# Performance work log

Hardware: AMD Instinct MI355X
Metric: run time of the kernel (lower is better)

The kernel has to match this reference:

```python
import jax, jax.numpy as jnp
import numpy as np
import math

D_MODEL = 1024
N_HEADS = 16
D_K = D_MODEL // N_HEADS
B, L = 4, 2048


def setup_inputs() -> dict:
    key = jax.random.key(0)
    ks = jax.random.split(key, 11)
    s = 1.0 / math.sqrt(D_MODEL)
    inp = {
        "queries": jax.random.normal(ks[0], (B, L, D_MODEL), jnp.float32),
        "keys": jax.random.normal(ks[1], (B, L, D_MODEL), jnp.float32),
        "values": jax.random.normal(ks[2], (B, L, D_MODEL), jnp.float32),
        "Wq": jax.random.normal(ks[3], (D_MODEL, D_MODEL), jnp.float32) * s,
        "bq": jax.random.normal(ks[4], (D_MODEL,), jnp.float32) * s,
        "Wk": jax.random.normal(ks[5], (D_MODEL, D_MODEL), jnp.float32) * s,
        "bk": jax.random.normal(ks[6], (D_MODEL,), jnp.float32) * s,
        "Wv": jax.random.normal(ks[7], (D_MODEL, D_MODEL), jnp.float32) * s,
        "bv": jax.random.normal(ks[8], (D_MODEL,), jnp.float32) * s,
        "Wo": jax.random.normal(ks[9], (D_MODEL, D_MODEL), jnp.float32) * s,
        "bo": jax.random.normal(ks[10], (D_MODEL,), jnp.float32) * s,
    }
    return inp


def _heads(x):
    b, l, _ = x.shape
    return x.reshape(b, l, N_HEADS, D_K).transpose(0, 2, 1, 3)  # (B,H,L,Dk)


def reference(queries, keys, values, Wq, bq, Wk, bk, Wv, bv, Wo, bo):
    Q = _heads(queries @ Wq.T + bq)
    K = _heads(keys @ Wk.T + bk)
    V = _heads(values @ Wv.T + bv)
    scores = jnp.einsum("bhqd,bhkd->bhqk", Q, K) / math.sqrt(D_K)
    t = jnp.arange(L, dtype=scores.dtype)
    time_bias = -0.1 * jnp.abs(t[None, :] - t[:, None])  # (L,L)
    attn = jax.nn.softmax(scores + time_bias[None, None], axis=-1)
    out = jnp.einsum("bhqk,bhkd->bhqd", attn, V)
    out = out.transpose(0, 2, 1, 3).reshape(queries.shape[0], L, D_MODEL)
    return out @ Wo.T + bo
```

## Files before the change

### kernel.cpp

```cpp
#include <hip/hip_runtime.h>
#include <hip/hip_bf16.h>
#include <stdint.h>

typedef __bf16 bf16x8 __attribute__((ext_vector_type(8)));
typedef float f32x4 __attribute__((ext_vector_type(4)));

__device__ __forceinline__ uint16_t f2bf(float f){
  uint32_t u = __builtin_bit_cast(uint32_t, f);
  u += 0x7fffu + ((u >> 16) & 1u);
  return (uint16_t)(u >> 16);
}

__device__ __forceinline__ void gld_lds16(const void* g, void* l){
  __builtin_amdgcn_global_load_lds((const __attribute__((address_space(1))) void*)g,
                                   (__attribute__((address_space(3))) void*)l, 16, 0, 0);
}

__global__ void convert_f32_bf16(const float* __restrict__ s, uint16_t* __restrict__ d, int n4){
  int i = blockIdx.x * blockDim.x + threadIdx.x;
  if (i >= n4) return;
  float4 v = ((const float4*)s)[i];
  ushort4 o;
  o.x = f2bf(v.x); o.y = f2bf(v.y); o.z = f2bf(v.z); o.w = f2bf(v.w);
  ((ushort4*)d)[i] = o;
}

__launch_bounds__(256, 2)
__global__ void gemm_bt(const uint16_t* __restrict__ A, const uint16_t* __restrict__ W,
                        const float* __restrict__ bias, void* __restrict__ out, int mode,
                        float oscale)
{
  __shared__ uint16_t As[128 * 64];
  __shared__ uint16_t Ws[128 * 64];
  const int tid = threadIdx.x;
  const int wave = tid >> 6, lane = tid & 63;
  const int g = lane >> 4, li = lane & 15;
  const int m0 = blockIdx.x * 128, n0 = blockIdx.y * 128;
  const int wr = (wave >> 1) * 64, wc = (wave & 1) * 64;

  f32x4 acc[4][4];
#pragma unroll
  for (int m = 0; m < 4; m++)
#pragma unroll
    for (int n = 0; n < 4; n++) acc[m][n] = f32x4{0.f, 0.f, 0.f, 0.f};

  const uint16_t* Asrc[4];
  const uint16_t* Wsrc[4];
  int cid[4];
#pragma unroll
  for (int j = 0; j < 4; j++) {
    cid[j] = j * 256 + tid;
    int row = cid[j] >> 3, c = cid[j] & 7;
    int sc = c ^ (row & 7);
    Asrc[j] = A + (size_t)(m0 + row) * 1024 + sc * 8;
    Wsrc[j] = W + (size_t)(n0 + row) * 1024 + sc * 8;
  }

  for (int k0 = 0; k0 < 1024; k0 += 64) {
#pragma unroll
    for (int j = 0; j < 4; j++) {
      gld_lds16(Asrc[j] + k0, (char*)As + cid[j] * 16);
      gld_lds16(Wsrc[j] + k0, (char*)Ws + cid[j] * 16);
    }
    __syncthreads();

#pragma unroll
    for (int kh = 0; kh < 2; kh++) {
      bf16x8 a[4], bfr[4];
#pragma unroll
      for (int m = 0; m < 4; m++) {
        int row = wr + m * 16 + li;
        int ch = (kh * 4 + g) ^ (row & 7);
        a[m] = *(const bf16x8*)((const char*)As + row * 128 + ch * 16);
      }
#pragma unroll
      for (int n = 0; n < 4; n++) {
        int row = wc + n * 16 + li;
        int ch = (kh * 4 + g) ^ (row & 7);
        bfr[n] = *(const bf16x8*)((const char*)Ws + row * 128 + ch * 16);
      }
#pragma unroll
      for (int m = 0; m < 4; m++)
#pragma unroll
        for (int n = 0; n < 4; n++)
          acc[m][n] = __builtin_amdgcn_mfma_f32_16x16x32_bf16(a[m], bfr[n], acc[m][n], 0, 0, 0);
    }
    __syncthreads();
  }

  if (mode == 0) {
    uint16_t* O = (uint16_t*)out;
#pragma unroll
    for (int n = 0; n < 4; n++) {
      int col = n0 + wc + n * 16 + li;
      float bv = bias[col];
#pragma unroll
      for (int m = 0; m < 4; m++) {
        int row = m0 + wr + m * 16 + g * 4;
#pragma unroll
        for (int r = 0; r < 4; r++)
          O[(size_t)(row + r) * 1024 + col] = f2bf((acc[m][n][r] + bv) * oscale);
      }
    }
  } else if (mode == 2) {
    uint16_t* O = (uint16_t*)out;
#pragma unroll
    for (int n = 0; n < 4; n++) {
      int col = n0 + wc + n * 16 + li;
      float bv = bias[col];
#pragma unroll
      for (int m = 0; m < 4; m++) {
        int mg = m0 + wr + m * 16 + g * 4;
        int bidx = mg >> 11;
        int l = mg & 2047;
        ushort4 pk;
        pk.x = f2bf(acc[m][n][0] + bv);
        pk.y = f2bf(acc[m][n][1] + bv);
        pk.z = f2bf(acc[m][n][2] + bv);
        pk.w = f2bf(acc[m][n][3] + bv);
        *(ushort4*)(O + ((size_t)bidx * 1024 + col) * 2048 + l) = pk;
      }
    }
  } else {
    float* O = (float*)out;
#pragma unroll
    for (int n = 0; n < 4; n++) {
      int col = n0 + wc + n * 16 + li;
      float bv = bias[col];
#pragma unroll
      for (int m = 0; m < 4; m++) {
        int row = m0 + wr + m * 16 + g * 4;
#pragma unroll
        for (int r = 0; r < 4; r++)
          O[(size_t)(row + r) * 1024 + col] = acc[m][n][r] + bv;
      }
    }
  }
}

__launch_bounds__(256, 2)
__global__ void flash_attn(const uint16_t* __restrict__ Qw, const uint16_t* __restrict__ Kw,
                           const uint16_t* __restrict__ Vt, uint16_t* __restrict__ Ow)
{
  __shared__ uint16_t Ks[64 * 64];
  __shared__ uint16_t Vs[64 * 64];
  __shared__ uint16_t Ps[4][16 * 64];

  const float C2 = 0.14426950408889635f;
  const float C3 = 20.1977305724455f;

  const int tid = threadIdx.x;
  const int wave = tid >> 6, lane = tid & 63;
  const int g = lane >> 4, li = lane & 15;
  const int q0 = blockIdx.x * 64;
  const int bh = blockIdx.y;
  const int b = bh >> 4, h = bh & 15;

  const uint16_t* Qp = Qw + (size_t)(b * 2048 + q0 + wave * 16 + li) * 1024 + h * 64 + g * 8;
  bf16x8 qf0 = *(const bf16x8*)Qp;
  bf16x8 qf1 = *(const bf16x8*)(Qp + 32);

  float l_r[4] = {0.f, 0.f, 0.f, 0.f};
  f32x4 o[4];
#pragma unroll
  for (int nd = 0; nd < 4; nd++) o[nd] = f32x4{0.f, 0.f, 0.f, 0.f};

  const int cid0 = tid, cid1 = 256 + tid;
  const int kr0 = cid0 >> 3, c0 = cid0 & 7;
  const int kr1 = cid1 >> 3, c1 = cid1 & 7;
  const int sc0 = c0 ^ (kr0 & 7), sc1 = c1 ^ (kr1 & 7);

  const uint16_t* Kb0 = Kw + (size_t)(b * 2048 + kr0) * 1024 + h * 64 + sc0 * 8;
  const uint16_t* Kb1 = Kw + (size_t)(b * 2048 + kr1) * 1024 + h * 64 + sc1 * 8;
  const uint16_t* Vb0 = Vt + (size_t)(bh * 64 + kr0) * 2048 + sc0 * 8;
  const uint16_t* Vb1 = Vt + (size_t)(bh * 64 + kr1) * 2048 + sc1 * 8;

  const int kv_lo = (q0 >= 256) ? (q0 - 256) : 0;
  const int kv_hi = (q0 + 320 <= 2048) ? (q0 + 320) : 2048;
  const int tq0 = q0 + wave * 16 + g * 4;

  for (int kv0 = kv_lo; kv0 < kv_hi; kv0 += 64) {
    gld_lds16(Kb0 + (size_t)kv0 * 1024, (char*)Ks + cid0 * 16);
    gld_lds16(Kb1 + (size_t)kv0 * 1024, (char*)Ks + cid1 * 16);
    gld_lds16(Vb0 + kv0, (char*)Vs + cid0 * 16);
    gld_lds16(Vb1 + kv0, (char*)Vs + cid1 * 16);
    __syncthreads();

    float p[4][4];
#pragma unroll
    for (int n = 0; n < 4; n++) {
      int kr = n * 16 + li;
      bf16x8 bk0 = *(const bf16x8*)((const char*)Ks + kr * 128 + ((g ^ (kr & 7)) << 4));
      bf16x8 bk1 = *(const bf16x8*)((const char*)Ks + kr * 128 + (((4 + g) ^ (kr & 7)) << 4));
      f32x4 s = f32x4{0.f, 0.f, 0.f, 0.f};
      s = __builtin_amdgcn_mfma_f32_16x16x32_bf16(qf0, bk0, s, 0, 0, 0);
      s = __builtin_amdgcn_mfma_f32_16x16x32_bf16(qf1, bk1, s, 0, 0, 0);
      float dtb = (float)(tq0 - (kv0 + n * 16 + li));
#pragma unroll
      for (int r = 0; r < 4; r++) {
        float e = exp2f((s[r] - C3) - C2 * fabsf(dtb + (float)r));
        p[n][r] = e;
        l_r[r] += e;
      }
    }

#pragma unroll
    for (int n = 0; n < 4; n++)
#pragma unroll
      for (int r = 0; r < 4; r++) {
        int prow = g * 4 + r;
        int c = n * 16 + li;
        Ps[wave][prow * 64 + ((((c >> 3) ^ (prow & 7))) << 3) + (c & 7)] = f2bf(p[n][r]);
      }

    bf16x8 pa0 = *(const bf16x8*)((const char*)Ps[wave] + li * 128 + ((g ^ (li & 7)) << 4));
    bf16x8 pa1 = *(const bf16x8*)((const char*)Ps[wave] + li * 128 + (((4 + g) ^ (li & 7)) << 4));
#pragma unroll
    for (int nd = 0; nd < 4; nd++) {
      int vr = nd * 16 + li;
      bf16x8 vb0 = *(const bf16x8*)((const char*)Vs + vr * 128 + ((g ^ (vr & 7)) << 4));
      bf16x8 vb1 = *(const bf16x8*)((const char*)Vs + vr * 128 + (((4 + g) ^ (vr & 7)) << 4));
      o[nd] = __builtin_amdgcn_mfma_f32_16x16x32_bf16(pa0, vb0, o[nd], 0, 0, 0);
      o[nd] = __builtin_amdgcn_mfma_f32_16x16x32_bf16(pa1, vb1, o[nd], 0, 0, 0);
    }
    __syncthreads();
  }

#pragma unroll
  for (int r = 0; r < 4; r++) {
    float l = l_r[r];
    l += __shfl_xor(l, 1);
    l += __shfl_xor(l, 2);
    l += __shfl_xor(l, 4);
    l += __shfl_xor(l, 8);
    float inv = 1.0f / l;
    int qg = b * 2048 + q0 + wave * 16 + g * 4 + r;
#pragma unroll
    for (int nd = 0; nd < 4; nd++)
      Ow[(size_t)qg * 1024 + h * 64 + nd * 16 + li] = f2bf(o[nd][r] * inv);
  }
}

extern "C" void kernel_launch(void* const* d_in, const int* in_sizes, int n_in,
                              void* d_out, int out_size, void* d_ws, size_t ws_size,
                              hipStream_t stream) {
  const float* q  = (const float*)d_in[0];
  const float* k  = (const float*)d_in[1];
  const float* v  = (const float*)d_in[2];
  const float* Wq = (const float*)d_in[3];
  const float* bq = (const float*)d_in[4];
  const float* Wk = (const float*)d_in[5];
  const float* bk = (const float*)d_in[6];
  const float* Wv = (const float*)d_in[7];
  const float* bv = (const float*)d_in[8];
  const float* Wo = (const float*)d_in[9];
  const float* bo = (const float*)d_in[10];

  const size_t NX = (size_t)8192 * 1024;
  const size_t NW = (size_t)1024 * 1024;

  uint16_t* Xb  = (uint16_t*)d_ws;
  uint16_t* Wb  = Xb + NX;
  uint16_t* Vtw = Wb + NW;
  uint16_t* Aws = Xb;
  uint16_t* Qws = (uint16_t*)d_out;
  uint16_t* Kws = Qws + NX;

  const int n4x = (int)(NX / 4);
  const int n4w = (int)(NW / 4);

  dim3 ggrid(64, 8);
  const float qscale = 0.18033688011112042f;

  convert_f32_bf16<<<n4x / 256, 256, 0, stream>>>(q, Xb, n4x);
  convert_f32_bf16<<<n4w / 256, 256, 0, stream>>>(Wq, Wb, n4w);
  gemm_bt<<<ggrid, 256, 0, stream>>>(Xb, Wb, bq, Qws, 0, qscale);

  convert_f32_bf16<<<n4x / 256, 256, 0, stream>>>(k, Xb, n4x);
  convert_f32_bf16<<<n4w / 256, 256, 0, stream>>>(Wk, Wb, n4w);
  gemm_bt<<<ggrid, 256, 0, stream>>>(Xb, Wb, bk, Kws, 0, 1.0f);

  convert_f32_bf16<<<n4x / 256, 256, 0, stream>>>(v, Xb, n4x);
  convert_f32_bf16<<<n4w / 256, 256, 0, stream>>>(Wv, Wb, n4w);
  gemm_bt<<<ggrid, 256, 0, stream>>>(Xb, Wb, bv, Vtw, 2, 1.0f);

  flash_attn<<<dim3(32, 64), 256, 0, stream>>>(Qws, Kws, Vtw, Aws);

  convert_f32_bf16<<<n4w / 256, 256, 0, stream>>>(Wo, Wb, n4w);
  gemm_bt<<<ggrid, 256, 0, stream>>>(Aws, Wb, bo, d_out, 3, 1.0f);
}
```

Baseline: 313.6 us.

## Double-buffer GEMM LDS tiles and merge input/weight conversion launches

The GEMM now keeps two LDS buffers per operand and issues the global-to-LDS loads for the next K tile before computing on the current one. The aim is to overlap load latency with MFMA work and drop one barrier per iteration. Activation and weight f32-to-bf16 conversions are merged into a single launch to save launch overhead, and the manual rounding is replaced by the compiler's bf16 cast. Doubling LDS use may lower occupancy. With only one barrier per iteration, there is also a risk of overwriting the buffer still being read from the previous iteration, since no wait or barrier is visible before the next prefetch.

```diff
diff --git a/kernel.cpp b/kernel.cpp
--- a/kernel.cpp
+++ b/kernel.cpp
@@ -6,9 +6,8 @@
 typedef float f32x4 __attribute__((ext_vector_type(4)));
 
 __device__ __forceinline__ uint16_t f2bf(float f){
-  uint32_t u = __builtin_bit_cast(uint32_t, f);
-  u += 0x7fffu + ((u >> 16) & 1u);
-  return (uint16_t)(u >> 16);
+  __bf16 h = (__bf16)f;
+  return __builtin_bit_cast(uint16_t, h);
 }
 
 __device__ __forceinline__ void gld_lds16(const void* g, void* l){
@@ -16,9 +15,12 @@
                                    (__attribute__((address_space(3))) void*)l, 16, 0, 0);
 }
 
-__global__ void convert_f32_bf16(const float* __restrict__ s, uint16_t* __restrict__ d, int n4){
+__global__ void convert2(const float* __restrict__ s1, uint16_t* __restrict__ d1, int n4_1,
+                         const float* __restrict__ s2, uint16_t* __restrict__ d2, int n4_2){
   int i = blockIdx.x * blockDim.x + threadIdx.x;
-  if (i >= n4) return;
+  const float* s; uint16_t* d;
+  if (i < n4_1) { s = s1; d = d1; }
+  else { i -= n4_1; if (i >= n4_2) return; s = s2; d = d2; }
   float4 v = ((const float4*)s)[i];
   ushort4 o;
   o.x = f2bf(v.x); o.y = f2bf(v.y); o.z = f2bf(v.z); o.w = f2bf(v.w);
@@ -30,8 +32,8 @@
                         const float* __restrict__ bias, void* __restrict__ out, int mode,
                         float oscale)
 {
-  __shared__ uint16_t As[128 * 64];
-  __shared__ uint16_t Ws[128 * 64];
+  __shared__ uint16_t As[2][128 * 64];
+  __shared__ uint16_t Ws[2][128 * 64];
   const int tid = threadIdx.x;
   const int wave = tid >> 6, lane = tid & 63;
   const int g = lane >> 4, li = lane & 15;
@@ -56,14 +58,27 @@
     Wsrc[j] = W + (size_t)(n0 + row) * 1024 + sc * 8;
   }
 
-  for (int k0 = 0; k0 < 1024; k0 += 64) {
-#pragma unroll
-    for (int j = 0; j < 4; j++) {
-      gld_lds16(Asrc[j] + k0, (char*)As + cid[j] * 16);
-      gld_lds16(Wsrc[j] + k0, (char*)Ws + cid[j] * 16);
-    }
-    __syncthreads();
-
+#pragma unroll
+  for (int j = 0; j < 4; j++) {
+    gld_lds16(Asrc[j], (char*)As[0] + cid[j] * 16);
+    gld_lds16(Wsrc[j], (char*)Ws[0] + cid[j] * 16);
+  }
+  __syncthreads();
+
+  for (int t = 0; t < 16; t++) {
+    const int cur = t & 1;
+    if (t < 15) {
+      const int k1 = (t + 1) * 64;
+      const int nxt = cur ^ 1;
+#pragma unroll
+      for (int j = 0; j < 4; j++) {
+        gld_lds16(Asrc[j] + k1, (char*)As[nxt] + cid[j] * 16);
+        gld_lds16(Wsrc[j] + k1, (char*)Ws[nxt] + cid[j] * 16);
+      }
+    }
+
+    const char* Ab = (const char*)As[cur];
+    const char* Wb = (const char*)Ws[cur];
 #pragma unroll
     for (int kh = 0; kh < 2; kh++) {
       bf16x8 a[4], bfr[4];
@@ -71,13 +86,13 @@
       for (int m = 0; m < 4; m++) {
         int row = wr + m * 16 + li;
         int ch = (kh * 4 + g) ^ (row & 7);
-        a[m] = *(const bf16x8*)((const char*)As + row * 128 + ch * 16);
+        a[m] = *(const bf16x8*)(Ab + row * 128 + ch * 16);
       }
 #pragma unroll
       for (int n = 0; n < 4; n++) {
         int row = wc + n * 16 + li;
         int ch = (kh * 4 + g) ^ (row & 7);
-        bfr[n] = *(const bf16x8*)((const char*)Ws + row * 128 + ch * 16);
+        bfr[n] = *(const bf16x8*)(Wb + row * 128 + ch * 16);
       }
 #pragma unroll
       for (int m = 0; m < 4; m++)
@@ -268,24 +283,22 @@
 
   const int n4x = (int)(NX / 4);
   const int n4w = (int)(NW / 4);
+  const int gcv = (n4x + n4w) / 256;
 
   dim3 ggrid(64, 8);
   const float qscale = 0.18033688011112042f;
 
-  convert_f32_bf16<<<n4x / 256, 256, 0, stream>>>(q, Xb, n4x);
-  convert_f32_bf16<<<n4w / 256, 256, 0, stream>>>(Wq, Wb, n4w);
+  convert2<<<gcv, 256, 0, stream>>>(q, Xb, n4x, Wq, Wb, n4w);
   gemm_bt<<<ggrid, 256, 0, stream>>>(Xb, Wb, bq, Qws, 0, qscale);
 
-  convert_f32_bf16<<<n4x / 256, 256, 0, stream>>>(k, Xb, n4x);
-  convert_f32_bf16<<<n4w / 256, 256, 0, stream>>>(Wk, Wb, n4w);
+  convert2<<<gcv, 256, 0, stream>>>(k, Xb, n4x, Wk, Wb, n4w);
   gemm_bt<<<ggrid, 256, 0, stream>>>(Xb, Wb, bk, Kws, 0, 1.0f);
 
-  convert_f32_bf16<<<n4x / 256, 256, 0, stream>>>(v, Xb, n4x);
-  convert_f32_bf16<<<n4w / 256, 256, 0, stream>>>(Wv, Wb, n4w);
+  convert2<<<gcv, 256, 0, stream>>>(v, Xb, n4x, Wv, Wb, n4w);
   gemm_bt<<<ggrid, 256, 0, stream>>>(Xb, Wb, bv, Vtw, 2, 1.0f);
 
   flash_attn<<<dim3(32, 64), 256, 0, stream>>>(Qws, Kws, Vtw, Aws);
 
-  convert_f32_bf16<<<n4w / 256, 256, 0, stream>>>(Wo, Wb, n4w);
+  convert2<<<n4w / 256, 256, 0, stream>>>(Wo, Wb, n4w, (const float*)0, (uint16_t*)0, 0);
   gemm_bt<<<ggrid, 256, 0, stream>>>(Aws, Wb, bo, d_out, 3, 1.0f);
 }
```

Result: no change. 310.2 us (-1.1%).
